# Kernel tuning notes

Measured on AMD Instinct MI355X. Metric: run time of the kernel, lower is better.

Reference implementation:

```python
import jax, jax.numpy as jnp
import numpy as np
from jax import lax

# dims
B = 1024          # batch
C_IN = 8          # board feature planes
HW = 8            # board side
FN = 16           # filter_num
SEN, INT, OUT = 1024, 2048, 1024
TOT = SEN + INT + OUT            # 4096
CNN_OUT = sum((HW - k + 1) ** 2 for k in range(1, 9)) * FN  # 204*FN = 3264
NUM_OUT = 1968
LORA_R = 64
LORA_SCALE = 128.0 / LORA_R      # alpha / rank = 2.0
TIMESTEPS = 5
DENSITY = 0.3


def setup_inputs() -> dict:
    key = jax.random.key(0)
    ks = jax.random.split(key, 20)
    inp = {"x": jax.random.normal(ks[0], (B, HW, HW, C_IN), dtype=jnp.float32)}
    # conv bank: kernels 1..8, OIHW layout
    for i, k in enumerate(range(1, 9)):
        inp[f"conv_w{k}"] = jax.random.normal(ks[1 + i], (FN, C_IN, k, k), dtype=jnp.float32) * (1.0 / np.sqrt(C_IN * k * k))
    inp["conv_b"] = jnp.zeros((8, FN), dtype=jnp.float32)
    # recurrent weight with sparsity pattern (mask = W != 0, as in register_buffer('sparsity_mask', W_init != 0))
    Wd = jax.random.normal(ks[9], (TOT, TOT), dtype=jnp.float32) * 0.02
    mask = (jax.random.uniform(ks[10], (TOT, TOT)) < DENSITY).astype(jnp.float32)
    inp["W"] = Wd * mask
    inp["lora_A"] = jax.random.normal(ks[11], (TOT, LORA_R), dtype=jnp.float32) * 0.02
    inp["lora_B"] = jax.random.normal(ks[12], (LORA_R, TOT), dtype=jnp.float32) * 0.02
    inp["ip_w"] = jax.random.normal(ks[13], (CNN_OUT, SEN), dtype=jnp.float32) * (1.0 / np.sqrt(CNN_OUT))
    inp["ip_b"] = jnp.zeros((SEN,), dtype=jnp.float32)
    inp["out_w"] = jax.random.normal(ks[14], (OUT, NUM_OUT), dtype=jnp.float32) * (1.0 / np.sqrt(OUT))
    inp["out_b"] = jnp.zeros((NUM_OUT,), dtype=jnp.float32)
    return inp


def _forward(x, conv_w1, conv_w2, conv_w3, conv_w4, conv_w5, conv_w6, conv_w7, conv_w8,
             conv_b, W, lora_A, lora_B, ip_w, ip_b, out_w, out_b):
    xn = jnp.transpose(x, (0, 3, 1, 2))  # NHWC -> NCHW, as x.permute(0,3,1,2)
    feats = []
    for i, cw in enumerate([conv_w1, conv_w2, conv_w3, conv_w4, conv_w5, conv_w6, conv_w7, conv_w8]):
        y = lax.conv_general_dilated(xn, cw, (1, 1), 'VALID',
                                     dimension_numbers=('NCHW', 'OIHW', 'NCHW'))
        y = jax.nn.relu(y + conv_b[i][None, :, None, None])  # use_relu=True
        feats.append(y.reshape(y.shape[0], -1))
    feat = jnp.concatenate(feats, axis=1)  # [B, CNN_OUT]

    # effective W with LoRA + sparsity mask
    mask = (W != 0).astype(W.dtype)
    W_eff = (W + (lora_A @ lora_B) * LORA_SCALE) * mask

    E = feat @ ip_w + ip_b                           # input_proj (no dropout: drop_out=False)
    E_pad = jnp.pad(E, ((0, 0), (0, TOT - SEN)))     # E feeds only the sensory block

    # The nine block matmuls S@Wss + I@Wrs + O@Wos etc. equal slices of state @ W_eff.
    state = jnp.zeros((x.shape[0], TOT), dtype=W.dtype)
    for t in range(TIMESTEPS):
        nxt = state @ W_eff
        if t == 0:
            nxt = nxt + E_pad
        nxt = state + nxt          # use_residual=True
        state = jax.nn.relu(nxt)

    O_state = state[:, SEN + INT:]
    return O_state @ out_w + out_b


def reference(x, conv_w1, conv_w2, conv_w3, conv_w4, conv_w5, conv_w6, conv_w7, conv_w8,
              conv_b, W, lora_A, lora_B, ip_w, ip_b, out_w, out_b):
    return _forward(x, conv_w1, conv_w2, conv_w3, conv_w4, conv_w5, conv_w6, conv_w7, conv_w8,
                    conv_b, W, lora_A, lora_B, ip_w, ip_b, out_w, out_b)
```

## Files before the change

kernel.cpp:

```cpp
#include <hip/hip_runtime.h>
#include <stdint.h>

typedef unsigned short u16;
typedef __attribute__((ext_vector_type(8))) short bf16x8;
typedef __attribute__((ext_vector_type(4))) float f32x4;

__device__ __forceinline__ u16 f2bf(float f) {
  union { float f; uint32_t u; } v; v.f = f;
  uint32_t u = v.u;
  return (u16)((u + 0x7fffu + ((u >> 16) & 1u)) >> 16);
}

__device__ __forceinline__ void gl_lds16(const void* g, void* l) {
  __builtin_amdgcn_global_load_lds(
      (const __attribute__((address_space(1))) uint32_t*)g,
      (__attribute__((address_space(3))) uint32_t*)l, 16, 0, 0);
}

__constant__ int c_off[9] = {0, 1024, 1808, 2384, 2784, 3040, 3184, 3248, 3264};

__global__ __launch_bounds__(256)
void prep_all(const float* __restrict__ x, u16* __restrict__ Xb,
              const float* __restrict__ lA, u16* __restrict__ lAb,
              const float* __restrict__ ip_w, u16* __restrict__ ip_wt,
              const float* __restrict__ out_w, u16* __restrict__ out_wt,
              const float* __restrict__ lB, u16* __restrict__ lBt,
              const float* w1, const float* w2, const float* w3, const float* w4,
              const float* w5, const float* w6, const float* w7, const float* w8,
              const float* __restrict__ cb,
              u16* __restrict__ Wct, float* __restrict__ bias_c) {
  __shared__ float tile[64][65];
  int b = blockIdx.x;
  const int t = threadIdx.x;
  if (b < 512) {
    const int i = b * 256 + t;
    const float4 v = ((const float4*)x)[i];
    ((ushort4*)Xb)[i] = make_ushort4(f2bf(v.x), f2bf(v.y), f2bf(v.z), f2bf(v.w));
    return;
  }
  b -= 512;
  if (b < 256) {
    const int i = b * 256 + t;
    const float4 v = ((const float4*)lA)[i];
    ((ushort4*)lAb)[i] = make_ushort4(f2bf(v.x), f2bf(v.y), f2bf(v.z), f2bf(v.w));
    return;
  }
  b -= 256;
  if (b < 1392) {
    const float* src; u16* dst; int R, C, bx, by;
    if (b < 816)        { src = ip_w;  dst = ip_wt;  R = 3264; C = 1024; bx = b % 16; by = b / 16; }
    else if (b < 1328)  { b -= 816;  src = out_w; dst = out_wt; R = 1024; C = 1968; bx = b % 32; by = b / 32; }
    else                { b -= 1328; src = lB;    dst = lBt;    R = 64;   C = 4096; bx = b;      by = 0; }
    const int rb = by << 6, cbs = bx << 6;
    for (int i = 0; i < 16; ++i) {
      const int idx = t + (i << 8);
      const int r = idx >> 6, c = idx & 63;
      float v = 0.f;
      if (cbs + c < C) v = src[(size_t)(rb + r) * C + cbs + c];
      tile[r][c] = v;
    }
    __syncthreads();
    const int c = t & 63, q = t >> 6;
    u16* dcol = dst + (size_t)(cbs + c) * R + rb;
    for (int v4 = 0; v4 < 4; ++v4) {
      const int r0 = (q << 4) + (v4 << 2);
      *(ushort4*)(dcol + r0) = make_ushort4(
          f2bf(tile[r0][c]), f2bf(tile[r0 + 1][c]),
          f2bf(tile[r0 + 2][c]), f2bf(tile[r0 + 3][c]));
    }
    return;
  }
  const int o0 = (b - 1392) << 3;
  for (int i = t; i < 1024; i += 256)
    *(ushort4*)(Wct + (size_t)(o0 + (i >> 7)) * 512 + ((i & 127) << 2)) =
        make_ushort4(0, 0, 0, 0);
  __syncthreads();
  const float* ws[8] = {w1, w2, w3, w4, w5, w6, w7, w8};
  for (int rr = 0; rr < 8; ++rr) {
    const int o = o0 + rr;
    if (o >= 3264) {
      if (t == 0) bias_c[o] = 0.f;
      continue;
    }
    u16* row = Wct + (size_t)o * 512;
    int kidx = 0;
    while (o >= c_off[kidx + 1]) ++kidx;
    const int ks = kidx + 1;
    const int s  = 8 - kidx;
    const int r  = o - c_off[kidx];
    const int f   = r / (s * s);
    const int rem = r - f * s * s;
    const int oi  = rem / s;
    const int oj  = rem - oi * s;
    const float* w = ws[kidx] + (size_t)f * 8 * ks * ks;
    const int ne = 8 * ks * ks;
    for (int e = t; e < ne; e += 256) {
      const int c  = e / (ks * ks);
      const int er = e - c * ks * ks;
      const int di = er / ks;
      const int dj = er - di * ks;
      row[((oi + di) * 8 + (oj + dj)) * 8 + c] = f2bf(w[(c * ks + di) * ks + dj]);
    }
    if (t == 0) bias_c[o] = cb[kidx * 16 + f];
  }
}

template<int EPI, int NR>
__device__ __forceinline__
void gemm_body(char* lds,
               const u16* __restrict__ A, int lda,
               const u16* __restrict__ Bt, int ldb, int K,
               const float* __restrict__ bias,
               const float* __restrict__ st_in, int st_ld,
               float* __restrict__ outf, int outf_ld,
               u16* __restrict__ outb, int outb_ld, int nvalid,
               int mb, int nb, int stf_c0) {
  constexpr int BN = NR * 32;
  u16 (*As)[64 * 64] = reinterpret_cast<u16 (*)[64 * 64]>(lds);
  u16 (*Bs)[BN * 64] = reinterpret_cast<u16 (*)[BN * 64]>(lds + 2 * 64 * 64 * 2);
  const int t = threadIdx.x;
  const int w = t >> 6, lane = t & 63;
  const int m0 = (w & 1) << 5, n0 = (w >> 1) * (NR << 4);
  const int lr = lane & 15, lq = lane >> 4;

  f32x4 acc[2][NR] = {};
  const int nk = K >> 6;

  auto stage = [&](int kt, int buf) {
    const int kb = kt << 6;
#pragma unroll
    for (int i = 0; i < 2; ++i) {
      const int c   = (w << 7) + (i << 6) + lane;
      const int row = c >> 3;
      const int kg  = (c & 7) ^ (row & 7);
      gl_lds16(A + (size_t)(mb + row) * lda + kb + (kg << 3),
               (char*)As[buf] + c * 16);
    }
#pragma unroll
    for (int i = 0; i < NR; ++i) {
      const int c   = w * (NR * 64) + (i << 6) + lane;
      const int row = c >> 3;
      const int kg  = (c & 7) ^ (row & 7);
      gl_lds16(Bt + (size_t)(nb + row) * ldb + kb + (kg << 3),
               (char*)Bs[buf] + c * 16);
    }
  };

  stage(0, 0);
  for (int kt = 0; kt < nk; ++kt) {
    const int buf = kt & 1;
    __syncthreads();
    if (kt + 1 < nk) stage(kt + 1, buf ^ 1);
#pragma unroll
    for (int kk = 0; kk < 2; ++kk) {
      const int kg = (kk << 2) + lq;
      const int sw = (kg ^ (lr & 7)) << 3;
      bf16x8 af[2], bf[NR];
#pragma unroll
      for (int i = 0; i < 2; ++i)
        af[i] = *(const bf16x8*)&As[buf][(m0 + (i << 4) + lr) * 64 + sw];
#pragma unroll
      for (int j = 0; j < NR; ++j)
        bf[j] = *(const bf16x8*)&Bs[buf][(n0 + (j << 4) + lr) * 64 + sw];
#pragma unroll
      for (int i = 0; i < 2; ++i)
#pragma unroll
        for (int j = 0; j < NR; ++j)
          acc[i][j] = __builtin_amdgcn_mfma_f32_16x16x32_bf16(af[i], bf[j], acc[i][j], 0, 0, 0);
    }
  }

#pragma unroll
  for (int i = 0; i < 2; ++i) {
#pragma unroll
    for (int j = 0; j < NR; ++j) {
      const int cg = nb + n0 + (j << 4) + lr;
#pragma unroll
      for (int r = 0; r < 4; ++r) {
        const int rg = mb + m0 + (i << 4) + (lq << 2) + r;
        float v = acc[i][j][r];
        if (EPI == 0) {
          outf[(size_t)rg * outf_ld + cg] = v;
        } else if (EPI == 1) {
          v += st_in[(size_t)rg * st_ld + cg];
          v = v > 0.f ? v : 0.f;
          if (cg >= stf_c0) outf[(size_t)rg * outf_ld + cg] = v;
          outb[(size_t)rg * outb_ld + cg] = f2bf(v);
        } else if (EPI == 2) {
          if (cg < nvalid)
            outf[(size_t)rg * outf_ld + cg] = v + bias[cg];
        } else {
          v += bias[cg];
          v = v > 0.f ? v : 0.f;
          outb[(size_t)rg * outb_ld + cg] = f2bf(v);
        }
      }
    }
  }
}

template<int EPI, int NR>
__global__ __launch_bounds__(256)
void gemm128(const u16* __restrict__ A, int lda,
             const u16* __restrict__ Bt, int ldb, int K,
             const float* __restrict__ bias,
             const float* __restrict__ st_in, int st_ld,
             float* __restrict__ outf, int outf_ld,
             u16* __restrict__ outb, int outb_ld, int nvalid, int stf_c0) {
  __shared__ __align__(16) char lds[2 * 64 * 64 * 2 + 2 * NR * 32 * 64 * 2];
  gemm_body<EPI, NR>(lds, A, lda, Bt, ldb, K, bias, st_in, st_ld,
                     outf, outf_ld, outb, outb_ld, nvalid,
                     blockIdx.y << 6, blockIdx.x * (NR * 32), stf_c0);
}

__global__ __launch_bounds__(512)
void gemm512e1(const u16* __restrict__ A, int lda,
               const u16* __restrict__ Bt, int ldb, int K,
               const float* __restrict__ st_in, int st_ld,
               float* __restrict__ outf, int outf_ld,
               u16* __restrict__ outb, int outb_ld, int stf_c0) {
  __shared__ __align__(16) u16 As[2][64 * 64];
  __shared__ __align__(16) u16 Bs[2][128 * 64];
  const int t = threadIdx.x;
  const int w = t >> 6, lane = t & 63;
  const int mb = blockIdx.y << 6, nb = blockIdx.x << 7;
  const int m0 = (w & 1) << 5, n0 = (w >> 1) << 5;
  const int lr = lane & 15, lq = lane >> 4;

  f32x4 acc[2][2] = {};
  const int nk = K >> 6;

  auto stage = [&](int kt, int buf) {
    const int kb = kt << 6;
    {
      const int c   = t;
      const int row = c >> 3;
      const int kg  = (c & 7) ^ (row & 7);
      gl_lds16(A + (size_t)(mb + row) * lda + kb + (kg << 3),
               (char*)As[buf] + c * 16);
    }
#pragma unroll
    for (int i = 0; i < 2; ++i) {
      const int c   = (i << 9) + t;
      const int row = c >> 3;
      const int kg  = (c & 7) ^ (row & 7);
      gl_lds16(Bt + (size_t)(nb + row) * ldb + kb + (kg << 3),
               (char*)Bs[buf] + c * 16);
    }
  };

  stage(0, 0);
  for (int kt = 0; kt < nk; ++kt) {
    const int buf = kt & 1;
    __syncthreads();
    if (kt + 1 < nk) stage(kt + 1, buf ^ 1);
#pragma unroll
    for (int kk = 0; kk < 2; ++kk) {
      const int kg = (kk << 2) + lq;
      const int sw = (kg ^ (lr & 7)) << 3;
      bf16x8 af[2], bf[2];
#pragma unroll
      for (int i = 0; i < 2; ++i)
        af[i] = *(const bf16x8*)&As[buf][(m0 + (i << 4) + lr) * 64 + sw];
#pragma unroll
      for (int j = 0; j < 2; ++j)
        bf[j] = *(const bf16x8*)&Bs[buf][(n0 + (j << 4) + lr) * 64 + sw];
#pragma unroll
      for (int i = 0; i < 2; ++i)
#pragma unroll
        for (int j = 0; j < 2; ++j)
          acc[i][j] = __builtin_amdgcn_mfma_f32_16x16x32_bf16(af[i], bf[j], acc[i][j], 0, 0, 0);
    }
  }

#pragma unroll
  for (int i = 0; i < 2; ++i)
#pragma unroll
    for (int j = 0; j < 2; ++j) {
      const int cg = nb + n0 + (j << 4) + lr;
#pragma unroll
      for (int r = 0; r < 4; ++r) {
        const int rg = mb + m0 + (i << 4) + (lq << 2) + r;
        float v = acc[i][j][r] + st_in[(size_t)rg * st_ld + cg];
        v = v > 0.f ? v : 0.f;
        if (cg >= stf_c0) outf[(size_t)rg * outf_ld + cg] = v;
        outb[(size_t)rg * outb_ld + cg] = f2bf(v);
      }
    }
}

__global__ __launch_bounds__(256)
void weff_conv(const float* __restrict__ W, const u16* __restrict__ lBt,
               const u16* __restrict__ lAb, u16* __restrict__ Wt,
               const u16* __restrict__ Xb, const u16* __restrict__ Wct,
               const float* __restrict__ bias_c, u16* __restrict__ feat) {
  __shared__ __align__(16) char lds[49152];
  const int b = blockIdx.x;
  const int t = threadIdx.x;
  if (b < 416) {
    const int bx = b % 26, by = b / 26;
    gemm_body<3, 4>(lds, Xb, 512, Wct, 512, 512, bias_c, nullptr, 0,
                    nullptr, 0, feat, 3328, 3328, by << 6, bx << 7, 0);
    return;
  }
  u16*   As_ = (u16*)lds;
  u16*   Bs_ = (u16*)(lds + 8192);
  float* Wl  = (float*)(lds + 16384);
  u16*   Ct  = (u16*)(lds + 32768);
  const int b2 = b - 416;
  const int w = t >> 6, lane = t & 63;
  const int nb = (b2 & 63) << 6, kb = (b2 >> 6) << 6;
  const int m0 = (w & 1) << 5, n0 = (w >> 1) << 5;
  const int lr = lane & 15, lq = lane >> 4;

  for (int i = 0; i < 2; ++i) {
    const int c   = (w << 7) + (i << 6) + lane;
    const int row = c >> 3;
    const int kg  = (c & 7) ^ (row & 7);
    gl_lds16(lBt + (size_t)(nb + row) * 64 + (kg << 3), (char*)As_ + c * 16);
    gl_lds16(lAb + (size_t)(kb + row) * 64 + (kg << 3), (char*)Bs_ + c * 16);
  }
  for (int i = 0; i < 4; ++i) {
    const int c   = (w << 8) + (i << 6) + lane;
    const int row = c >> 4;
    const int cc  = (c & 15) ^ (row & 15);
    gl_lds16(W + (size_t)(kb + row) * 4096 + nb + (cc << 2), (char*)Wl + c * 16);
  }
  __syncthreads();

  f32x4 acc[2][2] = {};
  for (int kk = 0; kk < 2; ++kk) {
    const int kg = (kk << 2) + lq;
    const int sw = (kg ^ (lr & 7)) << 3;
    bf16x8 af[2], bf[2];
    for (int i = 0; i < 2; ++i)
      af[i] = *(const bf16x8*)&As_[(m0 + (i << 4) + lr) * 64 + sw];
    for (int j = 0; j < 2; ++j)
      bf[j] = *(const bf16x8*)&Bs_[(n0 + (j << 4) + lr) * 64 + sw];
    for (int i = 0; i < 2; ++i)
      for (int j = 0; j < 2; ++j)
        acc[i][j] = __builtin_amdgcn_mfma_f32_16x16x32_bf16(af[i], bf[j], acc[i][j], 0, 0, 0);
  }

  for (int i = 0; i < 2; ++i) {
    for (int j = 0; j < 2; ++j) {
      const int cg  = n0 + (j << 4) + lr;
      const int rg0 = m0 + (i << 4) + (lq << 2);
      const int ch  = (rg0 >> 2) ^ (cg & 15);
      const float4 wv4 = *(const float4*)&Wl[cg * 64 + (ch << 2)];
      const float wv[4] = {wv4.x, wv4.y, wv4.z, wv4.w};
      for (int r = 0; r < 4; ++r)
        Ct[(rg0 + r) * 68 + cg] =
            (wv[r] != 0.f) ? f2bf(wv[r] + 2.0f * acc[i][j][r]) : (u16)0;
    }
  }
  __syncthreads();

  const int row = t >> 2, kp = (t & 3) << 4;
  u16* dst = Wt + (size_t)(nb + row) * 4096 + kb + kp;
  const u16* src = &Ct[row * 68 + kp];
  for (int i = 0; i < 4; ++i)
    *(ushort4*)(dst + (i << 2)) = *(const ushort4*)(src + (i << 2));
}

__global__ __launch_bounds__(256)
void gemm_e(const u16* __restrict__ A, const u16* __restrict__ Bt,
            float* __restrict__ part) {
  __shared__ __align__(16) char lds[49152];
  const int z = blockIdx.z;
  const int k0 = z * 832;
  const int nk = (z == 3) ? 12 : 13;
  gemm_body<0, 4>(lds, A + k0, 3328, Bt + k0, 3264, nk << 6,
                  nullptr, nullptr, 0, part + ((size_t)z << 20), 1024,
                  nullptr, 0, 0, blockIdx.y << 6, blockIdx.x << 7, 0);
}

__global__ __launch_bounds__(256)
void gemm_p4(const u16* __restrict__ A, const u16* __restrict__ Bt,
             float* __restrict__ part) {
  __shared__ __align__(16) char lds[32768];
  const int z = blockIdx.z;
  gemm_body<0, 2>(lds, A + (z << 10), 4096, Bt + (z << 10), 4096, 1024,
                  nullptr, nullptr, 0, part + ((size_t)z << 20), 1024,
                  nullptr, 0, 0, blockIdx.y << 6, blockIdx.x << 6, 0);
}

__global__ __launch_bounds__(256)
void e_combine(const float* __restrict__ part, const float* __restrict__ bias,
               float* __restrict__ st_f, u16* __restrict__ st_b) {
  const int i = (blockIdx.x * 256 + threadIdx.x) << 2;
  const int row = i >> 12, col = i & 4095;
  if (col < 1024) {
    const int pi = (row << 10) + col;
    const float4 a = *(const float4*)&part[pi];
    const float4 b = *(const float4*)&part[1024 * 1024 + pi];
    const float4 c = *(const float4*)&part[2 * 1024 * 1024 + pi];
    const float4 d = *(const float4*)&part[3 * 1024 * 1024 + pi];
    const float4 bs = *(const float4*)&bias[col];
    float v[4] = {a.x + b.x + c.x + d.x + bs.x, a.y + b.y + c.y + d.y + bs.y,
                  a.z + b.z + c.z + d.z + bs.z, a.w + b.w + c.w + d.w + bs.w};
    u16 o[4];
    for (int r = 0; r < 4; ++r) {
      v[r] = v[r] > 0.f ? v[r] : 0.f;
      o[r] = f2bf(v[r]);
    }
    *(float4*)&st_f[i] = make_float4(v[0], v[1], v[2], v[3]);
    *(ushort4*)&st_b[i] = make_ushort4(o[0], o[1], o[2], o[3]);
  } else {
    *(float4*)&st_f[i] = make_float4(0.f, 0.f, 0.f, 0.f);
    *(ushort4*)&st_b[i] = make_ushort4(0, 0, 0, 0);
  }
}

__global__ __launch_bounds__(256)
void t4_combine(const float* __restrict__ part, const float* __restrict__ st_in,
                u16* __restrict__ st_b) {
  const int i = (blockIdx.x * 256 + threadIdx.x) << 2;
  const int r = i >> 10, c = i & 1023;
  const float4 a  = *(const float4*)&part[i];
  const float4 b  = *(const float4*)&part[(1 << 20) + i];
  const float4 cc = *(const float4*)&part[(2 << 20) + i];
  const float4 d  = *(const float4*)&part[(3 << 20) + i];
  const float4 s  = *(const float4*)&st_in[(size_t)r * 4096 + 3072 + c];
  float v[4] = {a.x + b.x + cc.x + d.x + s.x, a.y + b.y + cc.y + d.y + s.y,
                a.z + b.z + cc.z + d.z + s.z, a.w + b.w + cc.w + d.w + s.w};
  u16 o[4];
  for (int k = 0; k < 4; ++k) {
    v[k] = v[k] > 0.f ? v[k] : 0.f;
    o[k] = f2bf(v[k]);
  }
  *(ushort4*)&st_b[(size_t)r * 4096 + 3072 + c] = make_ushort4(o[0], o[1], o[2], o[3]);
}

extern "C" void kernel_launch(void* const* d_in, const int* in_sizes, int n_in,
                              void* d_out, int out_size, void* d_ws, size_t ws_size,
                              hipStream_t stream) {
  const float* x     = (const float*)d_in[0];
  const float* cw[8];
  for (int i = 0; i < 8; ++i) cw[i] = (const float*)d_in[1 + i];
  const float* convb = (const float*)d_in[9];
  const float* W     = (const float*)d_in[10];
  const float* lA    = (const float*)d_in[11];
  const float* lB    = (const float*)d_in[12];
  const float* ip_w  = (const float*)d_in[13];
  const float* ip_b  = (const float*)d_in[14];
  const float* out_w = (const float*)d_in[15];
  const float* out_b = (const float*)d_in[16];
  float* out = (float*)d_out;

  char* p = (char*)d_ws;
  u16* feat   = (u16*)p;  p += (size_t)1024 * 3328 * 2;
  u16* ip_wt  = (u16*)p;  p += (size_t)1024 * 3264 * 2;
  u16* out_wt = (u16*)p;  p += (size_t)2048 * 1024 * 2;
  u16* Wt     = (u16*)p;  p += (size_t)4096 * 4096 * 2;
  float* st_f[2];
  st_f[0] = (float*)p;    p += (size_t)1024 * 4096 * 4;
  st_f[1] = (float*)p;    p += (size_t)1024 * 4096 * 4;
  u16* st_b[2];
  st_b[0] = (u16*)p;      p += (size_t)1024 * 4096 * 2;
  st_b[1] = (u16*)p;      p += (size_t)1024 * 4096 * 2;

  char* q = (char*)st_f[1];
  u16* Xb       = (u16*)q;  q += (size_t)1024 * 512 * 2;
  u16* Wct      = (u16*)q;  q += (size_t)3328 * 512 * 2;
  float* bias_c = (float*)q; q += (size_t)3328 * 4;
  u16* lBt      = (u16*)q;  q += (size_t)4096 * 64 * 2;
  u16* lAb      = (u16*)q;  q += (size_t)4096 * 64 * 2;
  float* Epart  = (float*)st_f[1];
  float* Tpart  = (float*)st_f[0];

  prep_all<<<2576, 256, 0, stream>>>(x, Xb, lA, lAb, ip_w, ip_wt,
                                     out_w, out_wt, lB, lBt,
                                     cw[0], cw[1], cw[2], cw[3],
                                     cw[4], cw[5], cw[6], cw[7], convb,
                                     Wct, bias_c);

  weff_conv<<<4512, 256, 0, stream>>>(W, lBt, lAb, Wt, Xb, Wct, bias_c, feat);

  gemm_e<<<dim3(8, 16, 4), 256, 0, stream>>>(feat, ip_wt, Epart);
  e_combine<<<4096, 256, 0, stream>>>(Epart, ip_b, st_f[0], st_b[0]);

  gemm512e1<<<dim3(32, 16), 512, 0, stream>>>(st_b[0], 4096, Wt, 4096, 1024,
      st_f[0], 4096, st_f[1], 4096, st_b[1], 4096, 0);

  gemm128<1, 4><<<dim3(32, 16), 256, 0, stream>>>(st_b[1], 4096, Wt, 4096, 4096,
      nullptr, st_f[1], 4096, st_f[0], 4096, st_b[0], 4096, 4096, 0);
  gemm128<1, 4><<<dim3(32, 16), 256, 0, stream>>>(st_b[0], 4096, Wt, 4096, 4096,
      nullptr, st_f[0], 4096, st_f[1], 4096, st_b[1], 4096, 4096, 3072);

  gemm_p4<<<dim3(16, 16, 4), 256, 0, stream>>>(st_b[1],
      Wt + (size_t)3072 * 4096, Tpart);
  t4_combine<<<1024, 256, 0, stream>>>(Tpart, st_f[1], st_b[0]);

  gemm128<2, 2><<<dim3(32, 16), 256, 0, stream>>>(st_b[0] + 3072, 4096, out_wt, 1024, 1024,
      out_b, nullptr, 0, out, 1968, nullptr, 0, 1968, 0);
}
```

Measured before the change: 349.3 us.

## Replace split-K partial GEMMs and combine kernels with fused-epilogue GEMMs

```diff
diff --git a/kernel.cpp b/kernel.cpp
--- a/kernel.cpp
+++ b/kernel.cpp
@@ -189,9 +189,14 @@
         } else if (EPI == 2) {
           if (cg < nvalid)
             outf[(size_t)rg * outf_ld + cg] = v + bias[cg];
+        } else if (EPI == 3) {
+          v += bias[cg];
+          v = v > 0.f ? v : 0.f;
+          outb[(size_t)rg * outb_ld + cg] = f2bf(v);
         } else {
           v += bias[cg];
           v = v > 0.f ? v : 0.f;
+          outf[(size_t)rg * outf_ld + cg] = v;
           outb[(size_t)rg * outb_ld + cg] = f2bf(v);
         }
       }
@@ -211,6 +216,30 @@
   gemm_body<EPI, NR>(lds, A, lda, Bt, ldb, K, bias, st_in, st_ld,
                      outf, outf_ld, outb, outb_ld, nvalid,
                      blockIdx.y << 6, blockIdx.x * (NR * 32), stf_c0);
+}
+
+__global__ __launch_bounds__(256)
+void e_fused(const u16* __restrict__ feat, const u16* __restrict__ ip_wt,
+             const float* __restrict__ ip_b,
+             float* __restrict__ st_f, u16* __restrict__ st_b) {
+  __shared__ __align__(16) char lds[2 * 64 * 64 * 2 + 2 * 64 * 64 * 2];
+  const int bx = blockIdx.x, by = blockIdx.y;
+  if (bx < 16) {
+    gemm_body<4, 2>(lds, feat, 3328, ip_wt, 3264, 3264, ip_b, nullptr, 0,
+                    st_f, 4096, st_b, 4096, 0, by << 6, bx << 6, 0);
+    return;
+  }
+  const int t = threadIdx.x;
+  const int r  = (by << 6) + (t >> 2);
+  const int c0 = (bx << 6) + ((t & 3) << 4);
+  float* pf = st_f + (size_t)r * 4096 + c0;
+  u16*   pb = st_b + (size_t)r * 4096 + c0;
+  const float4  z4 = make_float4(0.f, 0.f, 0.f, 0.f);
+  const ushort4 zu = make_ushort4(0, 0, 0, 0);
+#pragma unroll
+  for (int i = 0; i < 4; ++i) *(float4*)(pf + (i << 2)) = z4;
+#pragma unroll
+  for (int i = 0; i < 4; ++i) *(ushort4*)(pb + (i << 2)) = zu;
 }
 
 __global__ __launch_bounds__(512)
@@ -361,75 +390,6 @@
   const u16* src = &Ct[row * 68 + kp];
   for (int i = 0; i < 4; ++i)
     *(ushort4*)(dst + (i << 2)) = *(const ushort4*)(src + (i << 2));
-}
-
-__global__ __launch_bounds__(256)
-void gemm_e(const u16* __restrict__ A, const u16* __restrict__ Bt,
-            float* __restrict__ part) {
-  __shared__ __align__(16) char lds[49152];
-  const int z = blockIdx.z;
-  const int k0 = z * 832;
-  const int nk = (z == 3) ? 12 : 13;
-  gemm_body<0, 4>(lds, A + k0, 3328, Bt + k0, 3264, nk << 6,
-                  nullptr, nullptr, 0, part + ((size_t)z << 20), 1024,
-                  nullptr, 0, 0, blockIdx.y << 6, blockIdx.x << 7, 0);
-}
-
-__global__ __launch_bounds__(256)
-void gemm_p4(const u16* __restrict__ A, const u16* __restrict__ Bt,
-             float* __restrict__ part) {
-  __shared__ __align__(16) char lds[32768];
-  const int z = blockIdx.z;
-  gemm_body<0, 2>(lds, A + (z << 10), 4096, Bt + (z << 10), 4096, 1024,
-                  nullptr, nullptr, 0, part + ((size_t)z << 20), 1024,
-                  nullptr, 0, 0, blockIdx.y << 6, blockIdx.x << 6, 0);
-}
-
-__global__ __launch_bounds__(256)
-void e_combine(const float* __restrict__ part, const float* __restrict__ bias,
-               float* __restrict__ st_f, u16* __restrict__ st_b) {
-  const int i = (blockIdx.x * 256 + threadIdx.x) << 2;
-  const int row = i >> 12, col = i & 4095;
-  if (col < 1024) {
-    const int pi = (row << 10) + col;
-    const float4 a = *(const float4*)&part[pi];
-    const float4 b = *(const float4*)&part[1024 * 1024 + pi];
-    const float4 c = *(const float4*)&part[2 * 1024 * 1024 + pi];
-    const float4 d = *(const float4*)&part[3 * 1024 * 1024 + pi];
-    const float4 bs = *(const float4*)&bias[col];
-    float v[4] = {a.x + b.x + c.x + d.x + bs.x, a.y + b.y + c.y + d.y + bs.y,
-                  a.z + b.z + c.z + d.z + bs.z, a.w + b.w + c.w + d.w + bs.w};
-    u16 o[4];
-    for (int r = 0; r < 4; ++r) {
-      v[r] = v[r] > 0.f ? v[r] : 0.f;
-      o[r] = f2bf(v[r]);
-    }
-    *(float4*)&st_f[i] = make_float4(v[0], v[1], v[2], v[3]);
-    *(ushort4*)&st_b[i] = make_ushort4(o[0], o[1], o[2], o[3]);
-  } else {
-    *(float4*)&st_f[i] = make_float4(0.f, 0.f, 0.f, 0.f);
-    *(ushort4*)&st_b[i] = make_ushort4(0, 0, 0, 0);
-  }
-}
-
-__global__ __launch_bounds__(256)
-void t4_combine(const float* __restrict__ part, const float* __restrict__ st_in,
-                u16* __restrict__ st_b) {
-  const int i = (blockIdx.x * 256 + threadIdx.x) << 2;
-  const int r = i >> 10, c = i & 1023;
-  const float4 a  = *(const float4*)&part[i];
-  const float4 b  = *(const float4*)&part[(1 << 20) + i];
-  const float4 cc = *(const float4*)&part[(2 << 20) + i];
-  const float4 d  = *(const float4*)&part[(3 << 20) + i];
-  const float4 s  = *(const float4*)&st_in[(size_t)r * 4096 + 3072 + c];
-  float v[4] = {a.x + b.x + cc.x + d.x + s.x, a.y + b.y + cc.y + d.y + s.y,
-                a.z + b.z + cc.z + d.z + s.z, a.w + b.w + cc.w + d.w + s.w};
-  u16 o[4];
-  for (int k = 0; k < 4; ++k) {
-    v[k] = v[k] > 0.f ? v[k] : 0.f;
-    o[k] = f2bf(v[k]);
-  }
-  *(ushort4*)&st_b[(size_t)r * 4096 + 3072 + c] = make_ushort4(o[0], o[1], o[2], o[3]);
 }
 
 extern "C" void kernel_launch(void* const* d_in, const int* in_sizes, int n_in,
@@ -466,8 +426,6 @@
   float* bias_c = (float*)q; q += (size_t)3328 * 4;
   u16* lBt      = (u16*)q;  q += (size_t)4096 * 64 * 2;
   u16* lAb      = (u16*)q;  q += (size_t)4096 * 64 * 2;
-  float* Epart  = (float*)st_f[1];
-  float* Tpart  = (float*)st_f[0];
 
   prep_all<<<2576, 256, 0, stream>>>(x, Xb, lA, lAb, ip_w, ip_wt,
                                      out_w, out_wt, lB, lBt,
@@ -477,8 +435,8 @@
 
   weff_conv<<<4512, 256, 0, stream>>>(W, lBt, lAb, Wt, Xb, Wct, bias_c, feat);
 
-  gemm_e<<<dim3(8, 16, 4), 256, 0, stream>>>(feat, ip_wt, Epart);
-  e_combine<<<4096, 256, 0, stream>>>(Epart, ip_b, st_f[0], st_b[0]);
+  e_fused<<<dim3(64, 16), 256, 0, stream>>>(feat, ip_wt, ip_b,
+                                            st_f[0], st_b[0]);
 
   gemm512e1<<<dim3(32, 16), 512, 0, stream>>>(st_b[0], 4096, Wt, 4096, 1024,
       st_f[0], 4096, st_f[1], 4096, st_b[1], 4096, 0);
@@ -488,9 +446,10 @@
   gemm128<1, 4><<<dim3(32, 16), 256, 0, stream>>>(st_b[0], 4096, Wt, 4096, 4096,
       nullptr, st_f[0], 4096, st_f[1], 4096, st_b[1], 4096, 4096, 3072);
 
-  gemm_p4<<<dim3(16, 16, 4), 256, 0, stream>>>(st_b[1],
-      Wt + (size_t)3072 * 4096, Tpart);
-  t4_combine<<<1024, 256, 0, stream>>>(Tpart, st_f[1], st_b[0]);
+  gemm128<1, 2><<<dim3(16, 16), 256, 0, stream>>>(st_b[1], 4096,
+      Wt + (size_t)3072 * 4096, 4096, 4096,
+      nullptr, st_f[1] + 3072, 4096, nullptr, 0,
+      st_b[0] + 3072, 4096, 4096, 1 << 30);
 
   gemm128<2, 2><<<dim3(32, 16), 256, 0, stream>>>(st_b[0] + 3072, 4096, out_wt, 1024, 1024,
       out_b, nullptr, 0, out, 1968, nullptr, 0, 1968, 0);
```

After: 372.8 us. 6.7% more time.
